# Kernel tuning notes

Measured on AMD Instinct MI355X. Metric: run time of the kernel, lower is better.

The kernel has to match this reference:

```python
import jax, jax.numpy as jnp
import numpy as np

D_MODEL = 1024
D_HID = 1408
N_SHARED = 2
N_ROUTED = 8
TOP_K = 2
B, S = 2, 1024
EPS = float(jnp.finfo(jnp.float32).eps)  # torch RMSNorm eps=None -> finfo eps


def setup_inputs() -> dict:
    key = jax.random.key(0)
    ks = jax.random.split(key, 8)
    b1 = 1.0 / np.sqrt(D_MODEL)  # uniform bound for W1 (1/sqrt(d_input))
    b2 = 1.0 / np.sqrt(D_MODEL)  # uniform bound for W2 (1/sqrt(d_output))
    return {
        "x": jax.random.normal(ks[0], (B, S, D_MODEL), dtype=jnp.float32),
        "norm_w": jnp.ones((D_MODEL,), dtype=jnp.float32),
        "Wr": jax.random.uniform(ks[1], (N_ROUTED, D_MODEL), minval=-b1, maxval=b1, dtype=jnp.float32),
        "Ws1": jax.random.uniform(ks[2], (N_SHARED, D_MODEL, D_HID), minval=-b1, maxval=b1, dtype=jnp.float32),
        "bs1": jnp.zeros((N_SHARED, 1, D_HID), dtype=jnp.float32),
        "Ws2": jax.random.uniform(ks[3], (N_SHARED, D_HID, D_MODEL), minval=-b2, maxval=b2, dtype=jnp.float32),
        "bs2": jnp.zeros((N_SHARED, 1, D_MODEL), dtype=jnp.float32),
        "W1": jax.random.uniform(ks[4], (N_ROUTED, D_MODEL, D_HID), minval=-b1, maxval=b1, dtype=jnp.float32),
        "b1": jnp.zeros((N_ROUTED, 1, D_HID), dtype=jnp.float32),
        "W2": jax.random.uniform(ks[5], (N_ROUTED, D_HID, D_MODEL), minval=-b2, maxval=b2, dtype=jnp.float32),
        "b2": jnp.zeros((N_ROUTED, 1, D_MODEL), dtype=jnp.float32),
    }


def _rmsnorm(x, w):
    ms = jnp.mean(jnp.square(x), axis=-1, keepdims=True)
    return x * jax.lax.rsqrt(ms + EPS) * w


def reference(x, norm_w, Wr, Ws1, bs1, Ws2, bs2, W1, b1, W2, b2):
    inputs = _rmsnorm(x, norm_w)  # (B,S,d)

    # Shared experts: sum over all shared experts of SwiGLU-FFN
    hs = jax.nn.silu(jnp.einsum("bsd,edh->besh", inputs, Ws1) + bs1[:, None])  # (B,E_s,S,h)
    shared_out = jnp.einsum("besh,ehd->bsd", hs, Ws2) + jnp.sum(bs2[:, None], axis=0)  # (B,S,d)

    # Router (no bias, ver V2: affinity = raw logits)
    raw_aff = jnp.einsum("bsd,ed->bse", inputs, Wr)  # (B,S,E)
    _, idx = jax.lax.top_k(raw_aff, TOP_K)  # (B,S,K)

    # Routed experts: dropout=0, so computing all experts then gathering outputs
    # equals the source's per-token weight-gather math.
    hr = jax.nn.silu(jnp.einsum("bsd,edh->bseh", inputs, W1) + b1[:, 0])  # (B,S,E,h)
    out_all = jnp.einsum("bseh,ehd->bsed", hr, W2) + b2[:, 0]  # (B,S,E,d)

    out_k = jnp.take_along_axis(out_all, idx[..., None], axis=2)  # (B,S,K,d)
    aff_k = jnp.take_along_axis(raw_aff, idx, axis=-1)  # (B,S,K)
    routed_out = jnp.einsum("bsk,bskd->bsd", aff_k, out_k)

    return x + shared_out + routed_out
```

## Files before the change

kernel.cpp:

```cpp
#include <hip/hip_runtime.h>
#include <hip/hip_bf16.h>
#include <stdint.h>


#define NTOK 2048
#define DM   1024
#define DH   1408
#define NGRP 10
#define EPSV 1.1920928955078125e-7f
#define MAXTILES 40
#define MAXSLOTS (MAXTILES * 256)
#define MT128 (MAXSLOTS / 128)

typedef __bf16 bf16x8 __attribute__((ext_vector_type(8)));
typedef float  f32x4  __attribute__((ext_vector_type(4)));
typedef unsigned short u16x8 __attribute__((ext_vector_type(8)));

__device__ __forceinline__ void async16(const void* g, void* l) {
  __builtin_amdgcn_global_load_lds(
      (const __attribute__((address_space(1))) unsigned*)g,
      (__attribute__((address_space(3))) unsigned*)l, 16, 0, 0);
}

__device__ __forceinline__ unsigned lds_off(const void* p) {
  return (unsigned)(unsigned long long)(const __attribute__((address_space(3))) char*)p;
}

__device__ __forceinline__ unsigned short f2bf(float f) {
  unsigned u = __builtin_bit_cast(unsigned, f);
  unsigned r = (u + 0x7FFFu + ((u >> 16) & 1u)) >> 16;
  return (unsigned short)r;
}
__device__ __forceinline__ float bf2f(unsigned short h) {
  unsigned u = ((unsigned)h) << 16;
  return __builtin_bit_cast(float, u);
}

__device__ __forceinline__ float4 ntload4(const float* p) {
  const f32x4* vp = (const f32x4*)p;
  f32x4 v = __builtin_nontemporal_load(vp);
  float4 r;
  r.x = v[0]; r.y = v[1]; r.z = v[2]; r.w = v[3];
  return r;
}

__device__ __forceinline__ int xcd_swizzle(int id, int nwg) {
  int q = nwg >> 3;
  return (id & 7) * q + (id >> 3);
}

__device__ __forceinline__ void transpose_role(
    const float* s, unsigned short* d, int C, int Kd, int k0, int n0,
    unsigned short* Lt, int tid) {
#pragma unroll
  for (int p = 0; p < 8; ++p) {
    int kr = p * 8 + (tid >> 5);
    int nc = (tid & 31) * 4;
    float4 v = ntload4(s + (size_t)(k0 + kr) * C + n0 + nc);
    int ncs = nc ^ ((kr >> 3) << 2);
    ushort4 u;
    u.x = f2bf(v.x); u.y = f2bf(v.y); u.z = f2bf(v.z); u.w = f2bf(v.w);
    *(ushort4*)(&Lt[kr * 132 + ncs]) = u;
  }
  __syncthreads();
#pragma unroll
  for (int p = 0; p < 4; ++p) {
    int chunk = p * 256 + tid;
    int n = chunk >> 3, kc = (chunk & 7) * 8;
    int nswz = n ^ ((chunk & 7) << 2);
    u16x8 uv;
#pragma unroll
    for (int j = 0; j < 8; ++j) uv[j] = Lt[(kc + j) * 132 + nswz];
    *(u16x8*)(d + (size_t)(n0 + n) * Kd + k0 + kc) = uv;
  }
}

__global__ __launch_bounds__(256) void prep_k(
    const float* __restrict__ Ws1, const float* __restrict__ W1,
    unsigned short* __restrict__ W1t,
    const float* __restrict__ x, const float* __restrict__ nw,
    const float* __restrict__ Wr, unsigned short* __restrict__ xb,
    int* __restrict__ idx2, float* __restrict__ gate2) {
  __shared__ unsigned short Lt[64 * 132];
  __shared__ float ps[4];
  __shared__ float pw[32];
  int bi = blockIdx.x;
  int tid = threadIdx.x;
  if (bi < 1760) {
    int z = bi / 176, rem = bi % 176, kb = rem / 11, nb = rem % 11;
    const float* s = (z < 2) ? Ws1 + (size_t)z * DM * DH : W1 + (size_t)(z - 2) * DM * DH;
    unsigned short* d = W1t + (size_t)z * DH * DM;
    transpose_role(s, d, DH, DM, kb * 64, nb * 128, Lt, tid);
    return;
  }
  int t = bi - 1760;
  const float4 v = *(const float4*)(x + (size_t)t * DM + tid * 4);
  float s = v.x * v.x + v.y * v.y + v.z * v.z + v.w * v.w;
#pragma unroll
  for (int o = 32; o; o >>= 1) s += __shfl_down(s, o);
  if ((tid & 63) == 0) ps[tid >> 6] = s;
  __syncthreads();
  float tot = ps[0] + ps[1] + ps[2] + ps[3];
  float r = rsqrtf(tot * (1.0f / (float)DM) + EPSV);
  const float4 wv = *(const float4*)(nw + tid * 4);
  float4 y;
  y.x = v.x * r * wv.x; y.y = v.y * r * wv.y; y.z = v.z * r * wv.z; y.w = v.w * r * wv.w;
  ushort4 u; u.x = f2bf(y.x); u.y = f2bf(y.y); u.z = f2bf(y.z); u.w = f2bf(y.w);
  *(ushort4*)(xb + (size_t)t * DM + tid * 4) = u;
  float pr[8];
#pragma unroll
  for (int e = 0; e < 8; ++e) {
    const float4 w4 = *(const float4*)(Wr + (size_t)e * DM + tid * 4);
    pr[e] = y.x * w4.x + y.y * w4.y + y.z * w4.z + y.w * w4.w;
  }
#pragma unroll
  for (int e = 0; e < 8; ++e)
#pragma unroll
    for (int o = 32; o; o >>= 1) pr[e] += __shfl_down(pr[e], o);
  if ((tid & 63) == 0) {
    int w = tid >> 6;
#pragma unroll
    for (int e = 0; e < 8; ++e) pw[w * 8 + e] = pr[e];
  }
  __syncthreads();
  if (tid == 0) {
    float af[8];
#pragma unroll
    for (int e = 0; e < 8; ++e) af[e] = pw[e] + pw[8 + e] + pw[16 + e] + pw[24 + e];
    int e1 = 0; float a1 = af[0];
#pragma unroll
    for (int e = 1; e < 8; ++e) if (af[e] > a1) { a1 = af[e]; e1 = e; }
    int e2 = -1; float a2 = -3.4e38f;
#pragma unroll
    for (int e = 0; e < 8; ++e) if (e != e1 && af[e] > a2) { a2 = af[e]; e2 = e; }
    idx2[t * 2] = e1; idx2[t * 2 + 1] = e2;
    gate2[t * 2] = a1; gate2[t * 2 + 1] = a2;
  }
}

__global__ __launch_bounds__(256) void buildplace_k(
    const int* __restrict__ idx2, const float* __restrict__ gate2,
    const float* __restrict__ bs1, const float* __restrict__ b1,
    const float* __restrict__ bs2, const float* __restrict__ b2,
    int* __restrict__ tile_group, int* __restrict__ tok_list,
    float* __restrict__ gate_list, int* __restrict__ slot_of,
    float* __restrict__ b1p, float* __restrict__ b2p) {
  __shared__ int cnt_s[8], base_s[8], fill_s[8];
  int tid = threadIdx.x;
  if (tid < 8) { cnt_s[tid] = 0; fill_s[tid] = 0; }
  __syncthreads();
  for (int t = tid; t < NTOK; t += 256) {
    atomicAdd(&cnt_s[idx2[2 * t]], 1);
    atomicAdd(&cnt_s[idx2[2 * t + 1]], 1);
  }
  __syncthreads();
  if (tid == 0) {
    int tile = 16;
    for (int e = 0; e < 8; ++e) {
      base_s[e] = tile * 256;
      tile += (cnt_s[e] + 255) >> 8;
    }
    for (int i = 0; i < 16; ++i) tile_group[i] = i >> 3;
    int tt = 16;
    for (int e = 0; e < 8; ++e) {
      int nt = (cnt_s[e] + 255) >> 8;
      for (int i = 0; i < nt; ++i) tile_group[tt++] = 2 + e;
    }
    for (; tt < MAXTILES; ++tt) tile_group[tt] = -1;
  }
  for (int s = tid; s < MAXSLOTS; s += 256) {
    int tok; float gv;
    if (s < 2048)      { tok = s;        gv = 1.f; }
    else if (s < 4096) { tok = s - 2048; gv = 1.f; }
    else               { tok = -1;       gv = 0.f; }
    tok_list[s] = tok; gate_list[s] = gv;
  }
  for (int i = tid; i < NGRP * DH; i += 256) {
    int g = i / DH, j = i % DH;
    b1p[i] = (g < 2) ? bs1[g * DH + j] : b1[(g - 2) * DH + j];
  }
  for (int i = tid; i < NGRP * DM; i += 256) {
    int g = i >> 10, j = i & (DM - 1);
    b2p[i] = (g < 2) ? bs2[g * DM + j] : b2[(g - 2) * DM + j];
  }
  __syncthreads();
  for (int t = tid; t < NTOK; t += 256) {
#pragma unroll
    for (int k = 0; k < 2; ++k) {
      int e = idx2[t * 2 + k];
      int pos = atomicAdd(&fill_s[e], 1);
      int slot = base_s[e] + pos;
      tok_list[slot] = t;
      gate_list[slot] = gate2[t * 2 + k];
      slot_of[t * 2 + k] = slot;
    }
  }
}

#define DSR(dst, addr) asm volatile("ds_read_b128 %0, %1" : "=v"(dst) : "v"(addr))

template <int KD, int ND, bool FIRST>
__device__ __forceinline__ void gemm_body(
    int mt, int bn, char* smem,
    const unsigned short* __restrict__ A, const int* __restrict__ tok_list,
    const int* __restrict__ tile_group, const unsigned short* __restrict__ Bt,
    const float* __restrict__ biasP, const float* __restrict__ gate_list,
    unsigned short* __restrict__ Out) {
  constexpr int NK = KD / 32;
  int g = tile_group[mt >> 1];
  if (g < 0) return;
  int tid = threadIdx.x;
  unsigned short (*As)[128 * 32] = (unsigned short (*)[128 * 32])smem;
  unsigned short (*Bs)[128 * 32] = (unsigned short (*)[128 * 32])(smem + 16384);
  int* rows_s = (int*)(smem + 32768);
  float* gates_s = (float*)(smem + 33280);
  if (tid < 128) {
    if (FIRST) {
      int tok = tok_list[mt * 128 + tid];
      rows_s[tid] = tok < 0 ? 0 : tok;
    } else {
      gates_s[tid] = gate_list[mt * 128 + tid];
    }
  }
  __syncthreads();
  int drow = tid >> 2, schk = tid & 3;
  const unsigned short* aS[2];
  const unsigned short* bS[2];
#pragma unroll
  for (int p = 0; p < 2; ++p) {
    int rl = p * 64 + drow;
    int arow = FIRST ? rows_s[rl] : mt * 128 + rl;
    int sc = schk ^ ((rl >> 1) & 3);
    aS[p] = A + (size_t)arow * KD + sc * 8;
    bS[p] = Bt + ((size_t)g * ND + bn + rl) * KD + sc * 8;
  }
  int lane = tid & 63, w = tid >> 6;
  int wm = w >> 1, wn = w & 1;
  int lr = lane & 15, hi = lane >> 4;
  int aOff[4], bOff[4];
#pragma unroll
  for (int q = 0; q < 4; ++q) {
    int row = wm * 64 + q * 16 + lr;
    aOff[q] = row * 64 + ((hi ^ ((row >> 1) & 3)) << 4);
  }
#pragma unroll
  for (int nf = 0; nf < 4; ++nf) {
    int row = wn * 64 + nf * 16 + lr;
    bOff[nf] = row * 64 + ((hi ^ ((row >> 1) & 3)) << 4);
  }
  unsigned aBase[2] = {lds_off(&As[0][0]), lds_off(&As[1][0])};
  unsigned bBase[2] = {lds_off(&Bs[0][0]), lds_off(&Bs[1][0])};
  float bv[4];
#pragma unroll
  for (int nf = 0; nf < 4; ++nf) {
    int col = bn + wn * 64 + nf * 16 + lr;
    bv[nf] = biasP[g * (FIRST ? DH : DM) + col];
    asm volatile("" : "+v"(bv[nf]));
  }
  f32x4 acc[4][4];
#pragma unroll
  for (int q = 0; q < 4; ++q)
#pragma unroll
    for (int nf = 0; nf < 4; ++nf) acc[q][nf] = (f32x4){0.f, 0.f, 0.f, 0.f};
  auto stage = [&](int buf, int kt) {
#pragma unroll
    for (int p = 0; p < 2; ++p) {
      async16(aS[p] + kt * 32, (char*)&As[buf][0] + p * 4096 + tid * 16);
      async16(bS[p] + kt * 32, (char*)&Bs[buf][0] + p * 4096 + tid * 16);
    }
  };
  asm volatile("s_waitcnt vmcnt(0)" ::: "memory");
  __builtin_amdgcn_sched_barrier(0);
  stage(0, 0);
  __builtin_amdgcn_sched_barrier(0);
  int cur = 0;
  for (int kt = 0; kt < NK; ++kt) {
    if (kt + 1 < NK) {
      __builtin_amdgcn_sched_barrier(0);
      stage(cur ^ 1, kt + 1);
      __builtin_amdgcn_sched_barrier(0);
      asm volatile("s_waitcnt vmcnt(4)" ::: "memory");
      __builtin_amdgcn_sched_barrier(0);
    } else {
      asm volatile("s_waitcnt vmcnt(0)" ::: "memory");
      __builtin_amdgcn_sched_barrier(0);
    }
    asm volatile("s_barrier" ::: "memory");
    f32x4 ar[4], br[4];
#pragma unroll
    for (int q = 0; q < 4; ++q) DSR(ar[q], aBase[cur] + (unsigned)aOff[q]);
#pragma unroll
    for (int nf = 0; nf < 4; ++nf) DSR(br[nf], bBase[cur] + (unsigned)bOff[nf]);
    asm volatile("s_waitcnt lgkmcnt(0)" ::: "memory");
    __builtin_amdgcn_sched_barrier(0);
    __builtin_amdgcn_s_setprio(1);
#pragma unroll
    for (int q = 0; q < 4; ++q)
#pragma unroll
      for (int nf = 0; nf < 4; ++nf)
        acc[q][nf] = __builtin_amdgcn_mfma_f32_16x16x32_bf16(
            __builtin_bit_cast(bf16x8, ar[q]), __builtin_bit_cast(bf16x8, br[nf]),
            acc[q][nf], 0, 0, 0);
    __builtin_amdgcn_s_setprio(0);
    asm volatile("s_barrier" ::: "memory");
    cur ^= 1;
  }
#pragma unroll
  for (int nf = 0; nf < 4; ++nf) {
    int col = bn + wn * 64 + nf * 16 + lr;
#pragma unroll
    for (int q = 0; q < 4; ++q) {
      int rl = wm * 64 + q * 16 + hi * 4;
#pragma unroll
      for (int j = 0; j < 4; ++j) {
        float v = acc[q][nf][j] + bv[nf];
        if (FIRST) {
          v = v / (1.f + expf(-v));
          Out[(size_t)(mt * 128 + rl + j) * DH + col] = f2bf(v);
        } else {
          v *= gates_s[rl + j];
          Out[(size_t)(mt * 128 + rl + j) * DM + col] = f2bf(v);
        }
      }
    }
  }
}

__global__ __launch_bounds__(256, 4) void gemm1t_k(
    const unsigned short* __restrict__ A, const int* __restrict__ tok_list,
    const int* __restrict__ tile_group, const unsigned short* __restrict__ Bt,
    const float* __restrict__ b1p, unsigned short* __restrict__ Hb,
    const float* __restrict__ Ws2, const float* __restrict__ W2,
    unsigned short* __restrict__ W2t) {
  __shared__ char smem[33792];
  int bi = blockIdx.x;
  if (bi >= MT128 * 11) {
    int b2 = bi - MT128 * 11;
    int z = b2 / 176, rem = b2 % 176, kb = rem / 8, nb = rem % 8;
    const float* s = (z < 2) ? Ws2 + (size_t)z * DH * DM : W2 + (size_t)(z - 2) * DH * DM;
    unsigned short* d = W2t + (size_t)z * DM * DH;
    transpose_role(s, d, DM, DH, kb * 64, nb * 128, (unsigned short*)smem, threadIdx.x);
    return;
  }
  int wg = xcd_swizzle(bi, MT128 * 11);
  int mt = wg / 11, nb = wg % 11;
  gemm_body<DM, DH, true>(mt, nb * 128, smem, A, tok_list, tile_group, Bt, b1p, nullptr, Hb);
}

__global__ __launch_bounds__(256, 4) void gemm2_k(
    const unsigned short* __restrict__ A, const int* __restrict__ tok_list,
    const int* __restrict__ tile_group, const unsigned short* __restrict__ Bt,
    const float* __restrict__ b2p, const float* __restrict__ gate_list,
    unsigned short* __restrict__ Ob) {
  __shared__ char smem[33792];
  int wg = xcd_swizzle(blockIdx.x, MT128 * 8);
  int mt = wg >> 3, nb = wg & 7;
  gemm_body<DH, DM, false>(mt, nb * 128, smem, A, tok_list, tile_group, Bt, b2p, gate_list, Ob);
}

__global__ __launch_bounds__(256) void combine_k(
    const float* __restrict__ x, const unsigned short* __restrict__ O,
    const int* __restrict__ slot_of, float* __restrict__ out) {
  int t = blockIdx.x, tid = threadIdx.x;
  int d = tid * 4;
  int s0 = slot_of[t * 2], s1 = slot_of[t * 2 + 1];
  float4 xv = *(const float4*)(x + (size_t)t * DM + d);
  ushort4 a = *(const ushort4*)(O + (size_t)t * DM + d);
  ushort4 b = *(const ushort4*)(O + (size_t)(2048 + t) * DM + d);
  ushort4 c = *(const ushort4*)(O + (size_t)s0 * DM + d);
  ushort4 e = *(const ushort4*)(O + (size_t)s1 * DM + d);
  float4 o;
  o.x = xv.x + bf2f(a.x) + bf2f(b.x) + bf2f(c.x) + bf2f(e.x);
  o.y = xv.y + bf2f(a.y) + bf2f(b.y) + bf2f(c.y) + bf2f(e.y);
  o.z = xv.z + bf2f(a.z) + bf2f(b.z) + bf2f(c.z) + bf2f(e.z);
  o.w = xv.w + bf2f(a.w) + bf2f(b.w) + bf2f(c.w) + bf2f(e.w);
  *(float4*)(out + (size_t)t * DM + d) = o;
}

extern "C" void kernel_launch(void* const* d_in, const int* in_sizes, int n_in,
                              void* d_out, int out_size, void* d_ws, size_t ws_size,
                              hipStream_t stream) {
  const float* x   = (const float*)d_in[0];
  const float* nw  = (const float*)d_in[1];
  const float* Wr  = (const float*)d_in[2];
  const float* Ws1 = (const float*)d_in[3];
  const float* bs1 = (const float*)d_in[4];
  const float* Ws2 = (const float*)d_in[5];
  const float* bs2 = (const float*)d_in[6];
  const float* W1  = (const float*)d_in[7];
  const float* b1  = (const float*)d_in[8];
  const float* W2  = (const float*)d_in[9];
  const float* b2  = (const float*)d_in[10];
  float* out = (float*)d_out;

  char* ws = (char*)d_ws;
  size_t off = 0;
  auto alloc = [&](size_t n) {
    size_t r = off;
    off += (n + 255) & ~(size_t)255;
    return r;
  };
  unsigned short* XnB  = (unsigned short*)(ws + alloc((size_t)NTOK * DM * 2));
  unsigned short* W1t  = (unsigned short*)(ws + alloc((size_t)NGRP * DH * DM * 2));
  unsigned short* W2t  = (unsigned short*)(ws + alloc((size_t)NGRP * DM * DH * 2));
  unsigned short* Hb   = (unsigned short*)(ws + alloc((size_t)MAXSLOTS * DH * 2));
  unsigned short* Ob   = (unsigned short*)(ws + alloc((size_t)MAXSLOTS * DM * 2));
  int*   idx2      = (int*)(ws + alloc((size_t)NTOK * 2 * 4));
  float* gate2     = (float*)(ws + alloc((size_t)NTOK * 2 * 4));
  int*   tile_group= (int*)(ws + alloc(64 * 4));
  int*   tok_list  = (int*)(ws + alloc((size_t)MAXSLOTS * 4));
  float* gate_list = (float*)(ws + alloc((size_t)MAXSLOTS * 4));
  int*   slot_of   = (int*)(ws + alloc((size_t)NTOK * 2 * 4));
  float* b1p       = (float*)(ws + alloc((size_t)NGRP * DH * 4));
  float* b2p       = (float*)(ws + alloc((size_t)NGRP * DM * 4));

  prep_k<<<1760 + NTOK, 256, 0, stream>>>(Ws1, W1, W1t, x, nw, Wr, XnB, idx2, gate2);
  buildplace_k<<<1, 256, 0, stream>>>(idx2, gate2, bs1, b1, bs2, b2,
                                      tile_group, tok_list, gate_list, slot_of, b1p, b2p);
  gemm1t_k<<<MT128 * 11 + 1760, 256, 0, stream>>>(
      XnB, tok_list, tile_group, W1t, b1p, Hb, Ws2, W2, W2t);
  gemm2_k<<<MT128 * 8, 256, 0, stream>>>(
      Hb, tok_list, tile_group, W2t, b2p, gate_list, Ob);
  combine_k<<<NTOK, 256, 0, stream>>>(x, Ob, slot_of, out);
}
```

Measured before the change: 154.8 us.

## Use 256-row tiles with 512-thread blocks and a 4-stage LDS ring

Both grouped GEMMs move from 128x128 tiles on 256 threads to 256-row tiles on 512 threads: 256x256 for the first GEMM and 256x128 for the second. This raises reuse of each loaded A and B tile and cuts the number of blocks. The K loop is now a 4-slot LDS ring filled three stages ahead, with one barrier per iteration instead of two. The aim is to hide global-load latency and lower sync overhead. The cost is much more LDS per block (about 130 KB for the first GEMM), so only one block fits per CU. It also needs clamping and masking for the 1408-wide N edge, which leaves part of the last column tile idle.

```diff
diff --git a/kernel.cpp b/kernel.cpp
--- a/kernel.cpp
+++ b/kernel.cpp
@@ -8,9 +8,8 @@
 #define DH   1408
 #define NGRP 10
 #define EPSV 1.1920928955078125e-7f
-#define MAXTILES 40
-#define MAXSLOTS (MAXTILES * 256)
-#define MT128 (MAXSLOTS / 128)
+#define NTILES 40
+#define MAXSLOTS (NTILES * 256)
 
 typedef __bf16 bf16x8 __attribute__((ext_vector_type(8)));
 typedef float  f32x4  __attribute__((ext_vector_type(4)));
@@ -166,7 +165,7 @@
       int nt = (cnt_s[e] + 255) >> 8;
       for (int i = 0; i < nt; ++i) tile_group[tt++] = 2 + e;
     }
-    for (; tt < MAXTILES; ++tt) tile_group[tt] = -1;
+    for (; tt < NTILES; ++tt) tile_group[tt] = -1;
   }
   for (int s = tid; s < MAXSLOTS; s += 256) {
     int tok; float gv;
@@ -198,164 +197,180 @@
 }
 
 #define DSR(dst, addr) asm volatile("ds_read_b128 %0, %1" : "=v"(dst) : "v"(addr))
-
-template <int KD, int ND, bool FIRST>
+#define VMW(n) asm volatile("s_waitcnt vmcnt(" #n ")" ::: "memory")
+
+template <int KD, int ND, int BN, int WN_, int MF, int BL, bool FIRST>
 __device__ __forceinline__ void gemm_body(
-    int mt, int bn, char* smem,
+    int tile, int bn, char* smem,
     const unsigned short* __restrict__ A, const int* __restrict__ tok_list,
     const int* __restrict__ tile_group, const unsigned short* __restrict__ Bt,
     const float* __restrict__ biasP, const float* __restrict__ gate_list,
     unsigned short* __restrict__ Out) {
-  constexpr int NK = KD / 32;
-  int g = tile_group[mt >> 1];
+  constexpr int BM = 256, AL = 2, NF = 4;
+  constexpr int L = AL + BL;
+  constexpr int ASZ = BM * 64, BSZ = BN * 64, SLOT = ASZ + BSZ;
+  constexpr int H = KD / 32;
+  int g = tile_group[tile];
   if (g < 0) return;
   int tid = threadIdx.x;
-  unsigned short (*As)[128 * 32] = (unsigned short (*)[128 * 32])smem;
-  unsigned short (*Bs)[128 * 32] = (unsigned short (*)[128 * 32])(smem + 16384);
-  int* rows_s = (int*)(smem + 32768);
-  float* gates_s = (float*)(smem + 33280);
-  if (tid < 128) {
+  int* rows_s = (int*)(smem + 4 * SLOT);
+  float* gates_s = (float*)(smem + 4 * SLOT + 1024);
+  if (tid < 256) {
     if (FIRST) {
-      int tok = tok_list[mt * 128 + tid];
+      int tok = tok_list[tile * 256 + tid];
       rows_s[tid] = tok < 0 ? 0 : tok;
     } else {
-      gates_s[tid] = gate_list[mt * 128 + tid];
+      gates_s[tid] = gate_list[tile * 256 + tid];
     }
   }
   __syncthreads();
   int drow = tid >> 2, schk = tid & 3;
-  const unsigned short* aS[2];
-  const unsigned short* bS[2];
-#pragma unroll
-  for (int p = 0; p < 2; ++p) {
-    int rl = p * 64 + drow;
-    int arow = FIRST ? rows_s[rl] : mt * 128 + rl;
-    int sc = schk ^ ((rl >> 1) & 3);
-    aS[p] = A + (size_t)arow * KD + sc * 8;
-    bS[p] = Bt + ((size_t)g * ND + bn + rl) * KD + sc * 8;
+  const unsigned short* aS[AL];
+  const unsigned short* bS[BL];
+#pragma unroll
+  for (int p = 0; p < AL; ++p) {
+    int rl = p * 128 + drow;
+    int arow = FIRST ? rows_s[rl] : tile * 256 + rl;
+    aS[p] = A + (size_t)arow * KD + (schk ^ ((rl >> 1) & 3)) * 8;
+  }
+#pragma unroll
+  for (int p = 0; p < BL; ++p) {
+    int rl = p * 128 + drow;
+    int brow = bn + rl; if (brow > ND - 1) brow = ND - 1;
+    bS[p] = Bt + ((size_t)g * ND + brow) * KD + (schk ^ ((rl >> 1) & 3)) * 8;
   }
   int lane = tid & 63, w = tid >> 6;
-  int wm = w >> 1, wn = w & 1;
+  int wm = w / WN_, wn = w % WN_;
   int lr = lane & 15, hi = lane >> 4;
-  int aOff[4], bOff[4];
-#pragma unroll
-  for (int q = 0; q < 4; ++q) {
-    int row = wm * 64 + q * 16 + lr;
-    aOff[q] = row * 64 + ((hi ^ ((row >> 1) & 3)) << 4);
-  }
-#pragma unroll
-  for (int nf = 0; nf < 4; ++nf) {
+  int aOffB[MF], bOffB[NF];
+#pragma unroll
+  for (int q = 0; q < MF; ++q) {
+    int row = wm * (MF * 16) + q * 16 + lr;
+    aOffB[q] = row * 64 + ((hi ^ ((row >> 1) & 3)) << 4);
+  }
+#pragma unroll
+  for (int nf = 0; nf < NF; ++nf) {
     int row = wn * 64 + nf * 16 + lr;
-    bOff[nf] = row * 64 + ((hi ^ ((row >> 1) & 3)) << 4);
-  }
-  unsigned aBase[2] = {lds_off(&As[0][0]), lds_off(&As[1][0])};
-  unsigned bBase[2] = {lds_off(&Bs[0][0]), lds_off(&Bs[1][0])};
-  float bv[4];
-#pragma unroll
-  for (int nf = 0; nf < 4; ++nf) {
+    bOffB[nf] = ASZ + row * 64 + ((hi ^ ((row >> 1) & 3)) << 4);
+  }
+  unsigned ringB[4];
+#pragma unroll
+  for (int s = 0; s < 4; ++s) ringB[s] = lds_off(smem + s * SLOT);
+  float bv[NF];
+#pragma unroll
+  for (int nf = 0; nf < NF; ++nf) {
     int col = bn + wn * 64 + nf * 16 + lr;
-    bv[nf] = biasP[g * (FIRST ? DH : DM) + col];
+    int cidx = col < ND ? col : ND - 1;
+    bv[nf] = biasP[g * ND + cidx];
     asm volatile("" : "+v"(bv[nf]));
   }
-  f32x4 acc[4][4];
-#pragma unroll
-  for (int q = 0; q < 4; ++q)
-#pragma unroll
-    for (int nf = 0; nf < 4; ++nf) acc[q][nf] = (f32x4){0.f, 0.f, 0.f, 0.f};
-  auto stage = [&](int buf, int kt) {
-#pragma unroll
-    for (int p = 0; p < 2; ++p) {
-      async16(aS[p] + kt * 32, (char*)&As[buf][0] + p * 4096 + tid * 16);
-      async16(bS[p] + kt * 32, (char*)&Bs[buf][0] + p * 4096 + tid * 16);
-    }
+  f32x4 acc[MF][NF];
+#pragma unroll
+  for (int q = 0; q < MF; ++q)
+#pragma unroll
+    for (int nf = 0; nf < NF; ++nf) acc[q][nf] = (f32x4){0.f, 0.f, 0.f, 0.f};
+  auto stage = [&](int h) {
+    char* sb = smem + (h & 3) * SLOT;
+#pragma unroll
+    for (int p = 0; p < AL; ++p)
+      async16(aS[p] + h * 32, sb + p * 8192 + tid * 16);
+#pragma unroll
+    for (int p = 0; p < BL; ++p)
+      async16(bS[p] + h * 32, sb + ASZ + p * 8192 + tid * 16);
   };
-  asm volatile("s_waitcnt vmcnt(0)" ::: "memory");
+  VMW(0);
   __builtin_amdgcn_sched_barrier(0);
-  stage(0, 0);
+  stage(0); stage(1); stage(2);
   __builtin_amdgcn_sched_barrier(0);
-  int cur = 0;
-  for (int kt = 0; kt < NK; ++kt) {
-    if (kt + 1 < NK) {
+  for (int h = 0; h < H; ++h) {
+    if (h < H - 2) {
+      if constexpr (L == 4) VMW(8); else VMW(6);
+    } else if (h == H - 2) {
+      if constexpr (L == 4) VMW(4); else VMW(3);
+    } else {
+      VMW(0);
+    }
+    __builtin_amdgcn_sched_barrier(0);
+    asm volatile("s_barrier" ::: "memory");
+    if (h + 3 < H) {
       __builtin_amdgcn_sched_barrier(0);
-      stage(cur ^ 1, kt + 1);
+      stage(h + 3);
       __builtin_amdgcn_sched_barrier(0);
-      asm volatile("s_waitcnt vmcnt(4)" ::: "memory");
-      __builtin_amdgcn_sched_barrier(0);
-    } else {
-      asm volatile("s_waitcnt vmcnt(0)" ::: "memory");
-      __builtin_amdgcn_sched_barrier(0);
-    }
-    asm volatile("s_barrier" ::: "memory");
-    f32x4 ar[4], br[4];
-#pragma unroll
-    for (int q = 0; q < 4; ++q) DSR(ar[q], aBase[cur] + (unsigned)aOff[q]);
-#pragma unroll
-    for (int nf = 0; nf < 4; ++nf) DSR(br[nf], bBase[cur] + (unsigned)bOff[nf]);
+    }
+    f32x4 ar[MF], br[NF];
+    unsigned rb = ringB[h & 3];
+#pragma unroll
+    for (int q = 0; q < MF; ++q) DSR(ar[q], rb + (unsigned)aOffB[q]);
+#pragma unroll
+    for (int nf = 0; nf < NF; ++nf) DSR(br[nf], rb + (unsigned)bOffB[nf]);
     asm volatile("s_waitcnt lgkmcnt(0)" ::: "memory");
     __builtin_amdgcn_sched_barrier(0);
     __builtin_amdgcn_s_setprio(1);
 #pragma unroll
-    for (int q = 0; q < 4; ++q)
-#pragma unroll
-      for (int nf = 0; nf < 4; ++nf)
+    for (int q = 0; q < MF; ++q)
+#pragma unroll
+      for (int nf = 0; nf < NF; ++nf)
         acc[q][nf] = __builtin_amdgcn_mfma_f32_16x16x32_bf16(
             __builtin_bit_cast(bf16x8, ar[q]), __builtin_bit_cast(bf16x8, br[nf]),
             acc[q][nf], 0, 0, 0);
     __builtin_amdgcn_s_setprio(0);
-    asm volatile("s_barrier" ::: "memory");
-    cur ^= 1;
-  }
-#pragma unroll
-  for (int nf = 0; nf < 4; ++nf) {
+  }
+#pragma unroll
+  for (int nf = 0; nf < NF; ++nf) {
     int col = bn + wn * 64 + nf * 16 + lr;
-#pragma unroll
-    for (int q = 0; q < 4; ++q) {
-      int rl = wm * 64 + q * 16 + hi * 4;
-#pragma unroll
-      for (int j = 0; j < 4; ++j) {
-        float v = acc[q][nf][j] + bv[nf];
-        if (FIRST) {
-          v = v / (1.f + expf(-v));
-          Out[(size_t)(mt * 128 + rl + j) * DH + col] = f2bf(v);
-        } else {
-          v *= gates_s[rl + j];
-          Out[(size_t)(mt * 128 + rl + j) * DM + col] = f2bf(v);
+    if (col < ND) {
+#pragma unroll
+      for (int q = 0; q < MF; ++q) {
+        int rl = wm * (MF * 16) + q * 16 + hi * 4;
+#pragma unroll
+        for (int j = 0; j < 4; ++j) {
+          float v = acc[q][nf][j] + bv[nf];
+          if (FIRST) {
+            v = v / (1.f + expf(-v));
+            Out[(size_t)(tile * 256 + rl + j) * DH + col] = f2bf(v);
+          } else {
+            v *= gates_s[rl + j];
+            Out[(size_t)(tile * 256 + rl + j) * DM + col] = f2bf(v);
+          }
         }
       }
     }
   }
 }
 
-__global__ __launch_bounds__(256, 4) void gemm1t_k(
+__global__ __launch_bounds__(512, 2) void gemm1t_k(
     const unsigned short* __restrict__ A, const int* __restrict__ tok_list,
     const int* __restrict__ tile_group, const unsigned short* __restrict__ Bt,
     const float* __restrict__ b1p, unsigned short* __restrict__ Hb,
     const float* __restrict__ Ws2, const float* __restrict__ W2,
     unsigned short* __restrict__ W2t) {
-  __shared__ char smem[33792];
+  __shared__ char smem[4 * 32768 + 2048];
   int bi = blockIdx.x;
-  if (bi >= MT128 * 11) {
-    int b2 = bi - MT128 * 11;
+  if (bi >= 240) {
+    if (threadIdx.x >= 256) return;
+    int b2 = bi - 240;
     int z = b2 / 176, rem = b2 % 176, kb = rem / 8, nb = rem % 8;
     const float* s = (z < 2) ? Ws2 + (size_t)z * DH * DM : W2 + (size_t)(z - 2) * DH * DM;
     unsigned short* d = W2t + (size_t)z * DM * DH;
     transpose_role(s, d, DM, DH, kb * 64, nb * 128, (unsigned short*)smem, threadIdx.x);
     return;
   }
-  int wg = xcd_swizzle(bi, MT128 * 11);
-  int mt = wg / 11, nb = wg % 11;
-  gemm_body<DM, DH, true>(mt, nb * 128, smem, A, tok_list, tile_group, Bt, b1p, nullptr, Hb);
-}
-
-__global__ __launch_bounds__(256, 4) void gemm2_k(
+  int wg = xcd_swizzle(bi, 240);
+  int tile = wg / 6, bn = (wg % 6) * 256;
+  gemm_body<DM, DH, 256, 4, 8, 2, true>(tile, bn, smem, A, tok_list, tile_group,
+                                        Bt, b1p, nullptr, Hb);
+}
+
+__global__ __launch_bounds__(512, 2) void gemm2_k(
     const unsigned short* __restrict__ A, const int* __restrict__ tok_list,
     const int* __restrict__ tile_group, const unsigned short* __restrict__ Bt,
     const float* __restrict__ b2p, const float* __restrict__ gate_list,
     unsigned short* __restrict__ Ob) {
-  __shared__ char smem[33792];
-  int wg = xcd_swizzle(blockIdx.x, MT128 * 8);
-  int mt = wg >> 3, nb = wg & 7;
-  gemm_body<DH, DM, false>(mt, nb * 128, smem, A, tok_list, tile_group, Bt, b2p, gate_list, Ob);
+  __shared__ char smem[4 * 24576 + 2048];
+  int wg = xcd_swizzle(blockIdx.x, 320);
+  int tile = wg >> 3, bn = (wg & 7) * 128;
+  gemm_body<DH, DM, 128, 2, 4, 1, false>(tile, bn, smem, A, tok_list, tile_group,
+                                         Bt, b2p, gate_list, Ob);
 }
 
 __global__ __launch_bounds__(256) void combine_k(
@@ -417,9 +432,9 @@
   prep_k<<<1760 + NTOK, 256, 0, stream>>>(Ws1, W1, W1t, x, nw, Wr, XnB, idx2, gate2);
   buildplace_k<<<1, 256, 0, stream>>>(idx2, gate2, bs1, b1, bs2, b2,
                                       tile_group, tok_list, gate_list, slot_of, b1p, b2p);
-  gemm1t_k<<<MT128 * 11 + 1760, 256, 0, stream>>>(
+  gemm1t_k<<<240 + 1760, 512, 0, stream>>>(
       XnB, tok_list, tile_group, W1t, b1p, Hb, Ws2, W2, W2t);
-  gemm2_k<<<MT128 * 8, 256, 0, stream>>>(
+  gemm2_k<<<320, 512, 0, stream>>>(
       Hb, tok_list, tile_group, W2t, b2p, gate_list, Ob);
   combine_k<<<NTOK, 256, 0, stream>>>(x, Ob, slot_of, out);
 }
```

Result: slower. 169.0 us (+9.2%).
